# Kernel tuning notes

Hardware: AMD Instinct MI355X
Metric: run time of the kernel (lower is better)

The kernel has to match this reference:

```python
import jax, jax.numpy as jnp
import numpy as np

B, N, D = 2, 512, 256
H, HD = 4, 64  # hidden_dim=256 split across 4 heads (is_concat=True)
SLOPE = 0.2


def setup_inputs() -> dict:
    key = jax.random.key(0)
    ks = jax.random.split(key, 8)
    rn = lambda k, sh: jax.random.normal(k, sh, dtype=jnp.float32)
    return {
        "query": rn(ks[0], (B, N, D)),
        "key_in": rn(ks[1], (B, N, D)),
        "value": rn(ks[2], (B, N, D)),
        "w_q": rn(ks[3], (D, H * HD)) * 0.05,  # shared query/key projection (share_weights=True)
        "b_q": rn(ks[4], (H * HD,)) * 0.05,
        "w_v": rn(ks[5], (D, H * HD)) * 0.05,
        "b_v": rn(ks[6], (H * HD,)) * 0.05,
        "a": rn(ks[7], (HD,)) * 0.05,  # attention Linear(hd, 1, bias=False), shared across heads
    }


def reference(query, key_in, value, w_q, b_q, w_v, b_v, a):
    hq = (query @ w_q + b_q).reshape(B, N, H, HD)
    hk = (key_in @ w_q + b_q).reshape(B, N, H, HD)  # share_weights=True
    hv = (value @ w_v + b_v).reshape(B, N, H, HD)
    # torch repeat/repeat_interleave + view gives h[b,i,j] = hq[b,j] + hk[b,i]
    h = hq[:, None, :, :, :] + hk[:, :, None, :, :]  # [B, N, N, H, HD]
    e = jnp.einsum('bijhf,f->bijh', jax.nn.leaky_relu(h, SLOPE), a)
    e = jax.nn.softmax(e, axis=2)  # softmax over source nodes j (dropout is identity in eval)
    out = jnp.einsum('bijh,bjhf->bihf', e, hv).reshape(B, N, H * HD)  # is_concat
    h_prime = jax.nn.relu(out)
    return h_prime, e
```

## Files before the change

### kernel.cpp

```cpp
#include <hip/hip_runtime.h>


#define NB 2
#define NN 512
#define DD 256
#define NH 4
#define HDIM 64

typedef __attribute__((ext_vector_type(2))) float f32x2;

__device__ __forceinline__ f32x2 pk_fma(f32x2 a, f32x2 b, f32x2 c) {
    return __builtin_elementwise_fma(a, b, c);
}
__device__ __forceinline__ f32x2 pk_abs(f32x2 t) {
    return __builtin_elementwise_max(t, -t);
}

__global__ __launch_bounds__(256, 4) void proj_kernel(
    const float* __restrict__ q, const float* __restrict__ kin, const float* __restrict__ vin,
    const float* __restrict__ wq, const float* __restrict__ bq,
    const float* __restrict__ wv, const float* __restrict__ bv,
    float* __restrict__ hqt, float* __restrict__ hk, float* __restrict__ hv)
{
    const int m = blockIdx.z;
    const float* x    = (m == 0) ? q  : (m == 1) ? kin : vin;
    const float* w    = (m == 2) ? wv : wq;
    const float* bias = (m == 2) ? bv : bq;
    float* out        = (m == 0) ? hqt : (m == 1) ? hk : hv;

    const int r0 = blockIdx.x * 16;
    const int cb = blockIdx.y * 128;
    const int t  = threadIdx.x;

    __shared__ float xs[16][DD + 4];

    #pragma unroll
    for (int p = 0; p < 4; ++p) {
        const int idx = t + 256 * p;
        const int row = idx >> 6;
        const int kc  = idx & 63;
        const float4 v = *reinterpret_cast<const float4*>(&x[(size_t)(r0 + row) * DD + kc * 4]);
        *reinterpret_cast<float4*>(&xs[row][kc * 4]) = v;
    }
    __syncthreads();

    const int row0 = (t >> 5) * 2;
    const int c0   = (t & 31) * 4;

    const float4 b4 = *reinterpret_cast<const float4*>(&bias[cb + c0]);
    float acc[2][4];
    #pragma unroll
    for (int r = 0; r < 2; ++r) { acc[r][0]=b4.x; acc[r][1]=b4.y; acc[r][2]=b4.z; acc[r][3]=b4.w; }

    for (int kt = 0; kt < DD; kt += 4) {
        const float4 a0 = *reinterpret_cast<const float4*>(&xs[row0][kt]);
        const float4 a1 = *reinterpret_cast<const float4*>(&xs[row0 + 1][kt]);
        const float xa0[4] = {a0.x, a0.y, a0.z, a0.w};
        const float xa1[4] = {a1.x, a1.y, a1.z, a1.w};
        #pragma unroll
        for (int kk = 0; kk < 4; ++kk) {
            const float4 w4 = *reinterpret_cast<const float4*>(&w[(size_t)(kt + kk) * DD + cb + c0]);
            const float wv4[4] = {w4.x, w4.y, w4.z, w4.w};
            #pragma unroll
            for (int c = 0; c < 4; ++c) {
                acc[0][c] = fmaf(xa0[kk], wv4[c], acc[0][c]);
                acc[1][c] = fmaf(xa1[kk], wv4[c], acc[1][c]);
            }
        }
    }
    if (m == 0) {
        #pragma unroll
        for (int r = 0; r < 2; ++r) {
            const int rg = r0 + row0 + r;
            const int bb = rg >> 9, j = rg & 511;
            #pragma unroll
            for (int c = 0; c < 4; ++c) {
                const int col = cb + c0 + c;
                const int hh = col >> 6, f = col & 63;
                out[(((size_t)(bb * NH) + hh) * HDIM + f) * NN + j] = acc[r][c];
            }
        }
    } else {
        #pragma unroll
        for (int r = 0; r < 2; ++r) {
            float4 o; o.x = acc[r][0]; o.y = acc[r][1]; o.z = acc[r][2]; o.w = acc[r][3];
            *reinterpret_cast<float4*>(&out[(size_t)(r0 + row0 + r) * DD + cb + c0]) = o;
        }
    }
}

__global__ __launch_bounds__(512, 4) void attn_kernel(
    const float* __restrict__ hqt, const float* __restrict__ hk, const float* __restrict__ hv,
    const float* __restrict__ a, float* __restrict__ out_hp, float* __restrict__ out_e)
{
    const int t    = threadIdx.x;
    const int h    = blockIdx.x >> 7;
    const int rest = blockIdx.x & 127;
    const int b    = rest >> 6;
    const int i0   = (rest & 63) * 8;

    __shared__ float s[8][NN + 8];
    __shared__ float part[8][8][HDIM];

    const float* hk0 = hk + ((size_t)(b * NN) + i0) * DD + h * HDIM;

    {
        const int j = t;
        const float* hqb = hqt + (size_t)(b * NH + h) * HDIM * NN;
        f32x2 accu = {0.f, 0.f};
        f32x2 acc[8] = {};
        #pragma unroll
        for (int fc = 0; fc < 16; ++fc) {
            const int fo = fc * 4;
            const float q0 = hqb[(size_t)(fo + 0) * NN + j];
            const float q1 = hqb[(size_t)(fo + 1) * NN + j];
            const float q2 = hqb[(size_t)(fo + 2) * NN + j];
            const float q3 = hqb[(size_t)(fo + 3) * NN + j];
            const float4 a4 = *reinterpret_cast<const float4*>(a + fo);
            const f32x2 av[2] = {{a4.x, a4.y}, {a4.z, a4.w}};
            const f32x2 qv[2] = {{q0, q1}, {q2, q3}};
            #pragma unroll
            for (int ii = 0; ii < 8; ++ii) {
                const float4 kv = *reinterpret_cast<const float4*>(hk0 + ii * DD + fo);
                const f32x2 kk0 = {kv.x, kv.y}, kk1 = {kv.z, kv.w};
                acc[ii] = pk_fma(pk_abs(qv[0] + kk0), av[0], acc[ii]);
                acc[ii] = pk_fma(pk_abs(qv[1] + kk1), av[1], acc[ii]);
            }
            accu = pk_fma(qv[0], av[0], accu);
            accu = pk_fma(qv[1], av[1], accu);
        }
        const float su = 0.6f * (accu.x + accu.y);
        #pragma unroll
        for (int ii = 0; ii < 8; ++ii)
            s[ii][j] = fmaf(0.4f, acc[ii].x + acc[ii].y, su);
    }
    __syncthreads();

    {
        const int wv = t >> 6, lane = t & 63;
        float* row = &s[wv][0];
        float vals[8]; float mx = -1e30f;
        #pragma unroll
        for (int k2 = 0; k2 < 8; ++k2) { vals[k2] = row[lane + 64 * k2]; mx = fmaxf(mx, vals[k2]); }
        #pragma unroll
        for (int off = 32; off; off >>= 1) mx = fmaxf(mx, __shfl_xor(mx, off, 64));
        float sum = 0.f;
        #pragma unroll
        for (int k2 = 0; k2 < 8; ++k2) { vals[k2] = __expf(vals[k2] - mx); sum += vals[k2]; }
        #pragma unroll
        for (int off = 32; off; off >>= 1) sum += __shfl_xor(sum, off, 64);
        const float inv = 1.0f / sum;
        #pragma unroll
        for (int k2 = 0; k2 < 8; ++k2) row[lane + 64 * k2] = vals[k2] * inv;
    }
    __syncthreads();

    {
        float* oe = out_e + (((size_t)(b * NN) + i0) * NN) * NH + h;
        #pragma unroll
        for (int k2 = 0; k2 < 8; ++k2) {
            const int idx = t + 512 * k2;
            const int ii = idx >> 9;
            const int j  = idx & 511;
            oe[((size_t)ii * NN + j) * NH] = s[ii][j];
        }
    }

    {
        const int w    = t >> 6;
        const int lane = t & 63;
        const int jsub = lane >> 4;
        const int c0   = (lane & 15) * 4;
        const int jbase = w * 64;
        f32x2 acc0[8], acc1[8];
        #pragma unroll
        for (int ii = 0; ii < 8; ++ii) { acc0[ii] = f32x2{0.f, 0.f}; acc1[ii] = f32x2{0.f, 0.f}; }
        const float* hvb = hv + (size_t)(b * NN) * DD + h * HDIM + c0;
        #pragma unroll
        for (int it = 0; it < 16; ++it) {
            const int j = jbase + it * 4 + jsub;
            const float4 v4 = *reinterpret_cast<const float4*>(hvb + (size_t)j * DD);
            const f32x2 v0 = {v4.x, v4.y}, v1 = {v4.z, v4.w};
            #pragma unroll
            for (int ii = 0; ii < 8; ++ii) {
                const float e = s[ii][j];
                const f32x2 e2 = {e, e};
                acc0[ii] = pk_fma(e2, v0, acc0[ii]);
                acc1[ii] = pk_fma(e2, v1, acc1[ii]);
            }
        }
        #pragma unroll
        for (int ii = 0; ii < 8; ++ii) {
            #pragma unroll
            for (int off = 16; off <= 32; off <<= 1) {
                acc0[ii].x += __shfl_xor(acc0[ii].x, off, 64);
                acc0[ii].y += __shfl_xor(acc0[ii].y, off, 64);
                acc1[ii].x += __shfl_xor(acc1[ii].x, off, 64);
                acc1[ii].y += __shfl_xor(acc1[ii].y, off, 64);
            }
        }
        if (lane < 16) {
            #pragma unroll
            for (int ii = 0; ii < 8; ++ii) {
                float4 o; o.x = acc0[ii].x; o.y = acc0[ii].y; o.z = acc1[ii].x; o.w = acc1[ii].y;
                *reinterpret_cast<float4*>(&part[w][ii][c0]) = o;
            }
        }
    }
    __syncthreads();
    {
        const int ii = t >> 6, col = t & 63;
        float v = 0.f;
        #pragma unroll
        for (int w = 0; w < 8; ++w) v += part[w][ii][col];
        out_hp[((size_t)(b * NN) + i0 + ii) * DD + h * HDIM + col] = v > 0.f ? v : 0.f;
    }
}

extern "C" void kernel_launch(void* const* d_in, const int* in_sizes, int n_in,
                              void* d_out, int out_size, void* d_ws, size_t ws_size,
                              hipStream_t stream) {
    const float* q   = (const float*)d_in[0];
    const float* kin = (const float*)d_in[1];
    const float* vin = (const float*)d_in[2];
    const float* wq  = (const float*)d_in[3];
    const float* bq  = (const float*)d_in[4];
    const float* wv  = (const float*)d_in[5];
    const float* bv  = (const float*)d_in[6];
    const float* a   = (const float*)d_in[7];

    float* out_hp = (float*)d_out;
    float* out_e  = out_hp + (size_t)NB * NN * DD;

    float* hqt = (float*)d_ws;
    float* hk  = hqt + (size_t)NB * NN * DD;
    float* hv  = hk  + (size_t)NB * NN * DD;

    proj_kernel<<<dim3(64, 2, 3), 256, 0, stream>>>(q, kin, vin, wq, bq, wv, bv, hqt, hk, hv);
    attn_kernel<<<dim3(NB * 64 * NH), 512, 0, stream>>>(hqt, hk, hv, a, out_hp, out_e);
}
```

Measured before the change: 107.3 us.

## Retile projection GEMM with packed FMA and fuse softmax with e-store

The projection kernel moves to 32-row by 64-column tiles and uses packed two-wide FMAs. Each block now covers a single head, which simplifies the transposed hq store. In the attention kernel, the softmax normalization writes probabilities directly to out_e from registers, removing a barrier and a separate shared-memory read pass. The new tile doubles the shared-memory staging per block and halves the column reuse of each x row.

After: 106.6 us. Within noise of the previous version (-0.6%).

```diff
diff --git a/kernel.cpp b/kernel.cpp
--- a/kernel.cpp
+++ b/kernel.cpp
@@ -28,14 +28,14 @@
     const float* bias = (m == 2) ? bv : bq;
     float* out        = (m == 0) ? hqt : (m == 1) ? hk : hv;
 
-    const int r0 = blockIdx.x * 16;
-    const int cb = blockIdx.y * 128;
+    const int r0 = blockIdx.x * 32;
+    const int cb = blockIdx.y * 64;
     const int t  = threadIdx.x;
 
-    __shared__ float xs[16][DD + 4];
+    __shared__ float xs[32][DD + 4];
 
     #pragma unroll
-    for (int p = 0; p < 4; ++p) {
+    for (int p = 0; p < 8; ++p) {
         const int idx = t + 256 * p;
         const int row = idx >> 6;
         const int kc  = idx & 63;
@@ -44,47 +44,48 @@
     }
     __syncthreads();
 
-    const int row0 = (t >> 5) * 2;
-    const int c0   = (t & 31) * 4;
+    const int rp2 = (t >> 4) * 2;
+    const int c0  = (t & 15) * 4;
 
     const float4 b4 = *reinterpret_cast<const float4*>(&bias[cb + c0]);
-    float acc[2][4];
+    f32x2 acc[2][2];
     #pragma unroll
-    for (int r = 0; r < 2; ++r) { acc[r][0]=b4.x; acc[r][1]=b4.y; acc[r][2]=b4.z; acc[r][3]=b4.w; }
+    for (int rr = 0; rr < 2; ++rr) { acc[rr][0] = f32x2{b4.x, b4.y}; acc[rr][1] = f32x2{b4.z, b4.w}; }
 
     for (int kt = 0; kt < DD; kt += 4) {
-        const float4 a0 = *reinterpret_cast<const float4*>(&xs[row0][kt]);
-        const float4 a1 = *reinterpret_cast<const float4*>(&xs[row0 + 1][kt]);
+        const float4 a0 = *reinterpret_cast<const float4*>(&xs[rp2][kt]);
+        const float4 a1 = *reinterpret_cast<const float4*>(&xs[rp2 + 1][kt]);
         const float xa0[4] = {a0.x, a0.y, a0.z, a0.w};
         const float xa1[4] = {a1.x, a1.y, a1.z, a1.w};
         #pragma unroll
         for (int kk = 0; kk < 4; ++kk) {
             const float4 w4 = *reinterpret_cast<const float4*>(&w[(size_t)(kt + kk) * DD + cb + c0]);
-            const float wv4[4] = {w4.x, w4.y, w4.z, w4.w};
-            #pragma unroll
-            for (int c = 0; c < 4; ++c) {
-                acc[0][c] = fmaf(xa0[kk], wv4[c], acc[0][c]);
-                acc[1][c] = fmaf(xa1[kk], wv4[c], acc[1][c]);
-            }
+            const f32x2 wlo = {w4.x, w4.y}, whi = {w4.z, w4.w};
+            const f32x2 x0 = {xa0[kk], xa0[kk]};
+            const f32x2 x1 = {xa1[kk], xa1[kk]};
+            acc[0][0] = pk_fma(x0, wlo, acc[0][0]);
+            acc[0][1] = pk_fma(x0, whi, acc[0][1]);
+            acc[1][0] = pk_fma(x1, wlo, acc[1][0]);
+            acc[1][1] = pk_fma(x1, whi, acc[1][1]);
         }
     }
     if (m == 0) {
-        #pragma unroll
-        for (int r = 0; r < 2; ++r) {
-            const int rg = r0 + row0 + r;
+        const int hh = cb >> 6;
+        #pragma unroll
+        for (int rr = 0; rr < 2; ++rr) {
+            const int rg = r0 + rp2 + rr;
             const int bb = rg >> 9, j = rg & 511;
-            #pragma unroll
-            for (int c = 0; c < 4; ++c) {
-                const int col = cb + c0 + c;
-                const int hh = col >> 6, f = col & 63;
-                out[(((size_t)(bb * NH) + hh) * HDIM + f) * NN + j] = acc[r][c];
-            }
+            const float v4[4] = {acc[rr][0].x, acc[rr][0].y, acc[rr][1].x, acc[rr][1].y};
+            #pragma unroll
+            for (int cc = 0; cc < 4; ++cc)
+                out[(((size_t)(bb * NH) + hh) * HDIM + (c0 + cc)) * NN + j] = v4[cc];
         }
     } else {
         #pragma unroll
-        for (int r = 0; r < 2; ++r) {
-            float4 o; o.x = acc[r][0]; o.y = acc[r][1]; o.z = acc[r][2]; o.w = acc[r][3];
-            *reinterpret_cast<float4*>(&out[(size_t)(r0 + row0 + r) * DD + cb + c0]) = o;
+        for (int rr = 0; rr < 2; ++rr) {
+            const int rg = r0 + rp2 + rr;
+            float4 o; o.x = acc[rr][0].x; o.y = acc[rr][0].y; o.z = acc[rr][1].x; o.w = acc[rr][1].y;
+            *reinterpret_cast<float4*>(&out[(size_t)rg * DD + cb + c0]) = o;
         }
     }
 }
@@ -150,21 +151,16 @@
         #pragma unroll
         for (int off = 32; off; off >>= 1) sum += __shfl_xor(sum, off, 64);
         const float inv = 1.0f / sum;
-        #pragma unroll
-        for (int k2 = 0; k2 < 8; ++k2) row[lane + 64 * k2] = vals[k2] * inv;
-    }
-    __syncthreads();
-
-    {
-        float* oe = out_e + (((size_t)(b * NN) + i0) * NN) * NH + h;
+        float* oe = out_e + (((size_t)(b * NN) + i0 + wv) * NN) * NH + h;
         #pragma unroll
         for (int k2 = 0; k2 < 8; ++k2) {
-            const int idx = t + 512 * k2;
-            const int ii = idx >> 9;
-            const int j  = idx & 511;
-            oe[((size_t)ii * NN + j) * NH] = s[ii][j];
-        }
-    }
+            const int j = lane + 64 * k2;
+            const float p = vals[k2] * inv;
+            row[j] = p;
+            oe[(size_t)j * NH] = p;
+        }
+    }
+    __syncthreads();
 
     {
         const int w    = t >> 6;
@@ -236,6 +232,6 @@
     float* hk  = hqt + (size_t)NB * NN * DD;
     float* hv  = hk  + (size_t)NB * NN * DD;
 
-    proj_kernel<<<dim3(64, 2, 3), 256, 0, stream>>>(q, kin, vin, wq, bq, wv, bv, hqt, hk, hv);
+    proj_kernel<<<dim3(32, 4, 3), 256, 0, stream>>>(q, kin, vin, wq, bq, wv, bv, hqt, hk, hv);
     attn_kernel<<<dim3(NB * 64 * NH), 512, 0, stream>>>(hqt, hk, hv, a, out_hp, out_e);
 }
```
